# Kernel tuning notes

Measured on AMD Instinct MI355X. Metric: run time of the kernel, lower is better.

The kernel has to match this reference:

```python
import jax, jax.numpy as jnp
import numpy as np

N = 16384
H = 2048
E = 8
I_PER_E = 8192 // E  # expert_intermediate_size = 1024


def setup_inputs() -> dict:
    key = jax.random.key(0)
    k1, k2, k3, k4 = jax.random.split(key, 4)
    hidden_states = jax.random.normal(k1, (N, H), dtype=jnp.float32)
    # sort_idx is a permutation of [0, N): tokens sorted by expert assignment
    sort_idx = jax.random.permutation(k2, N).astype(jnp.int64)
    # kaiming_uniform_ with a=sqrt(5): bound = sqrt(6/((1+a^2)*fan_in)) = 1/sqrt(fan_in)
    bound = 1.0 / np.sqrt(H)
    gate_up_proj = jax.random.uniform(k3, (E, H, 2 * I_PER_E), dtype=jnp.float32,
                                      minval=-bound, maxval=bound)
    # original inits down_proj to zeros; use small random so backward is non-trivial
    down_proj = jax.random.normal(k4, (E, I_PER_E, H), dtype=jnp.float32) * 0.02
    return {"hidden_states": hidden_states, "sort_idx": sort_idx,
            "gate_up_proj": gate_up_proj, "down_proj": down_proj}


def reference(hidden_states, sort_idx, gate_up_proj, down_proj):
    n, h = hidden_states.shape
    e = gate_up_proj.shape[0]
    chunk = n // e
    # gather tokens into expert order: [E, chunk, H]
    sorted_x = hidden_states[sort_idx].reshape(e, chunk, h)
    # fused gate+up grouped GEMM: [E, chunk, 2*I/E]
    gu = jnp.einsum('ech,ehf->ecf', sorted_x, gate_up_proj)
    gate, up = jnp.split(gu, 2, axis=-1)
    activated = jax.nn.silu(gate) * up  # [E, chunk, I/E]
    sorted_out = jnp.einsum('eci,eih->ech', activated, down_proj).reshape(n, h)
    # scatter back: out[sort_idx] = sorted_out
    out = jnp.zeros((n, h), dtype=sorted_out.dtype).at[sort_idx].set(sorted_out)
    return out
```

## Files before the change

### kernel.cpp

```cpp
#include <hip/hip_runtime.h>
#include <hip/hip_bf16.h>

#define N_TOK 16384
#define H_DIM 2048
#define NE 8
#define CHUNK 2048
#define IPE 1024
#define F2 2048

typedef __bf16 bf16;
typedef bf16 bf16x8 __attribute__((ext_vector_type(8)));
typedef float f32x4 __attribute__((ext_vector_type(4)));

typedef __attribute__((address_space(1))) void gvoid;
typedef __attribute__((address_space(3))) void svoid;

__device__ __forceinline__ void gload_lds16(const void* g, void* l) {
  __builtin_amdgcn_global_load_lds((gvoid*)g, (svoid*)l, 16, 0, 0);
}
__device__ __forceinline__ f32x4 MF(bf16x8 a, bf16x8 b, f32x4 c) {
  return __builtin_amdgcn_mfma_f32_16x16x32_bf16(a, b, c, 0, 0, 0);
}

#define BAR() __builtin_amdgcn_s_barrier()
#define LGKM0() asm volatile("s_waitcnt lgkmcnt(0)" ::: "memory")
#define LGKM8() asm volatile("s_waitcnt lgkmcnt(8)" ::: "memory")
#define VM6() asm volatile("s_waitcnt vmcnt(6)" ::: "memory")
#define VM0() asm volatile("s_waitcnt vmcnt(0)" ::: "memory")
#define PRIO(x) __builtin_amdgcn_s_setprio(x)

__global__ __launch_bounds__(256) void k_gather(
    const float* __restrict__ x, const int* __restrict__ sidx,
    bf16* __restrict__ xs) {
  int row = blockIdx.x;
  int src = sidx[row];
  const float4* ip = (const float4*)(x + (size_t)src * H_DIM);
  int t = threadIdx.x;
  float4 f0 = ip[t * 2], f1 = ip[t * 2 + 1];
  bf16x8 v;
  v[0] = (bf16)f0.x; v[1] = (bf16)f0.y; v[2] = (bf16)f0.z; v[3] = (bf16)f0.w;
  v[4] = (bf16)f1.x; v[5] = (bf16)f1.y; v[6] = (bf16)f1.z; v[7] = (bf16)f1.w;
  *(bf16x8*)(xs + (size_t)row * H_DIM + t * 8) = v;
}

__global__ __launch_bounds__(256) void k_tr_w1(const float* __restrict__ in,
                                               bf16* __restrict__ out) {
  int e = blockIdx.z;
  int fB = blockIdx.x;
  int hB = blockIdx.y;
  __shared__ bf16 lds[64][68];
  int tx = threadIdx.x & 63;
  int ty = threadIdx.x >> 6;
  const float* ip = in + ((size_t)e * H_DIM + hB * 64) * F2;
  int scol = (tx < 32) ? (fB * 32 + tx) : (1024 + fB * 32 + (tx - 32));
#pragma unroll
  for (int p = 0; p < 16; ++p) {
    int hl = p * 4 + ty;
    lds[hl][tx] = (bf16)ip[(size_t)hl * F2 + scol];
  }
  __syncthreads();
  bf16* op = out + ((size_t)e * F2 + fB * 64) * H_DIM + hB * 64;
#pragma unroll
  for (int p = 0; p < 16; ++p) {
    int fl = p * 4 + ty;
    int g = fl >> 4, w = fl & 15;
    int lcol = ((g >> 1) << 4) + w + ((g & 1) << 5);
    op[(size_t)fl * H_DIM + tx] = lds[tx][lcol];
  }
}

__global__ __launch_bounds__(256) void k_tr_w2(const float* __restrict__ in,
                                               bf16* __restrict__ out) {
  int e = blockIdx.z;
  int hB = blockIdx.x;
  int iB = blockIdx.y;
  __shared__ bf16 lds[64][68];
  int tx = threadIdx.x & 63;
  int ty = threadIdx.x >> 6;
  const float* ip = in + (size_t)e * IPE * H_DIM + (size_t)iB * 64 * H_DIM + hB * 64;
#pragma unroll
  for (int p = 0; p < 16; ++p) {
    int il = p * 4 + ty;
    lds[il][tx] = (bf16)ip[(size_t)il * H_DIM + tx];
  }
  __syncthreads();
  bf16* op = out + (size_t)e * H_DIM * IPE + (size_t)hB * 64 * IPE + iB * 64;
#pragma unroll
  for (int p = 0; p < 16; ++p) {
    int hl = p * 4 + ty;
    op[(size_t)hl * IPE + tx] = lds[tx][hl];
  }
}

template <int KDIM, bool SILU>
__global__ __launch_bounds__(512) void k_gemm8(
    const bf16* __restrict__ Aptr, const bf16* __restrict__ Bptr,
    const int* __restrict__ sidx, bf16* __restrict__ act,
    float* __restrict__ fout) {
  extern __shared__ char smem[];
  const int tid = threadIdx.x, lane = tid & 63, wv = tid >> 6;
  const int wm = wv >> 2, wn = wv & 3;
  constexpr int NT = KDIM / 64;

  int swzwg = (blockIdx.x & 7) * (gridDim.x >> 3) + (blockIdx.x >> 3);
  const int e = swzwg >> 6, bm = (swzwg >> 3) & 7, bn = swzwg & 7;

  const char* Ab = (const char*)(Aptr + ((size_t)e * CHUNK + bm * 256) * KDIM);
  const char* Bb = (const char*)(Bptr + ((size_t)e * 2048 + bn * 256) * KDIM);

  const int L0 = wv * 1024 + lane * 16;
  const int lin0 = L0 ^ (((L0 >> 7) & 7) << 4);
  const int srow0 = lin0 >> 7, scolb = lin0 & 127;

  const int rA = lane & 15;
  const int swzr = (rA & 7) << 4;
  const int cb = (lane >> 4) * 16;

  f32x4 acc[8][4] = {};

  auto stage = [&](int buf, int mat, int half, int kt) {
    const char* gb = (mat == 0) ? Ab : Bb;
    char* ld = smem + buf * 65536 + mat * 32768 + half * 16384 + wv * 1024;
    size_t rb = (size_t)(half * 128 + srow0) * (KDIM * 2) + (size_t)kt * 128 + scolb;
    gload_lds16(gb + rb, ld);
    gload_lds16(gb + rb + (size_t)64 * (KDIM * 2), ld + 8192);
  };
  auto ldA = [&](int buf, int mi, int ks) {
    int lin = ((mi * 16 + rA) << 7) + ks * 64 + cb;
    return *(const bf16x8*)(smem + buf * 65536 + wm * 16384 + (lin ^ swzr));
  };
  auto ldB = [&](int buf, int ni, int ks) {
    int lin = (((wn & 1) * 64 + ni * 16 + rA) << 7) + ks * 64 + cb;
    return *(const bf16x8*)(smem + buf * 65536 + 32768 + (wn >> 1) * 16384 + (lin ^ swzr));
  };

  stage(0, 1, 0, 0); stage(0, 1, 1, 0); stage(0, 0, 0, 0); stage(0, 0, 1, 0);
  stage(1, 1, 0, 1); stage(1, 1, 1, 1); stage(1, 0, 0, 1);
  VM6();
  BAR();

  for (int t = 0; t < NT; ++t) {
    const int cur = t & 1, nxt = cur ^ 1;
    bf16x8 b0[4], b1[4], a0[4], a1[4], a2[4];
#pragma unroll
    for (int ni = 0; ni < 4; ++ni) { b0[ni] = ldB(cur, ni, 0); b1[ni] = ldB(cur, ni, 1); }
#pragma unroll
    for (int mi = 0; mi < 4; ++mi) a0[mi] = ldA(cur, mi, 0);
    if (t + 1 < NT) stage(nxt, 0, 1, t + 1);
    LGKM8();
    BAR();
    LGKM0();
    PRIO(1);
#pragma unroll
    for (int mi = 0; mi < 4; ++mi)
#pragma unroll
      for (int ni = 0; ni < 4; ++ni) acc[mi][ni] = MF(a0[mi], b0[ni], acc[mi][ni]);
    PRIO(0);
    BAR();
#pragma unroll
    for (int mi = 0; mi < 4; ++mi) a1[mi] = ldA(cur, mi, 1);
#pragma unroll
    for (int mi = 0; mi < 4; ++mi) a2[mi] = ldA(cur, 4 + mi, 0);
    if (t + 2 < NT) stage(cur, 1, 0, t + 2);
    BAR();
    LGKM0();
    PRIO(1);
#pragma unroll
    for (int mi = 0; mi < 4; ++mi)
#pragma unroll
      for (int ni = 0; ni < 4; ++ni) acc[mi][ni] = MF(a1[mi], b1[ni], acc[mi][ni]);
    PRIO(0);
    BAR();
#pragma unroll
    for (int mi = 0; mi < 4; ++mi) a0[mi] = ldA(cur, 4 + mi, 1);
    if (t + 2 < NT) stage(cur, 1, 1, t + 2);
    BAR();
    LGKM0();
    PRIO(1);
#pragma unroll
    for (int mi = 0; mi < 4; ++mi)
#pragma unroll
      for (int ni = 0; ni < 4; ++ni) acc[4 + mi][ni] = MF(a2[mi], b0[ni], acc[4 + mi][ni]);
    PRIO(0);
    BAR();
    if (t + 2 < NT) {
      stage(cur, 0, 0, t + 2);
      VM6();
    } else if (t + 1 < NT) {
      VM0();
    }
    BAR();
    PRIO(1);
#pragma unroll
    for (int mi = 0; mi < 4; ++mi)
#pragma unroll
      for (int ni = 0; ni < 4; ++ni) acc[4 + mi][ni] = MF(a0[mi], b1[ni], acc[4 + mi][ni]);
    PRIO(0);
    BAR();
  }

  if constexpr (SILU) {
    bf16* actp = act + ((size_t)e * CHUNK + bm * 256 + wm * 128) * IPE;
    const int r0 = (lane >> 4) * 4;
    const int c0 = bn * 128 + wn * 32 + (lane & 15);
#pragma unroll
    for (int mi = 0; mi < 8; ++mi)
#pragma unroll
      for (int p = 0; p < 2; ++p) {
        f32x4 g = acc[mi][2 * p], u = acc[mi][2 * p + 1];
#pragma unroll
        for (int r = 0; r < 4; ++r) {
          float gv = g[r];
          float a = gv / (1.f + __expf(-gv)) * u[r];
          actp[(size_t)(mi * 16 + r0 + r) * IPE + c0 + p * 16] = (bf16)a;
        }
      }
  } else {
    const int* sp = sidx + e * CHUNK + bm * 256 + wm * 128;
    const int r0 = (lane >> 4) * 4;
    const int c0 = bn * 256 + wn * 64 + (lane & 15);
#pragma unroll
    for (int mi = 0; mi < 8; ++mi)
#pragma unroll
      for (int r = 0; r < 4; ++r) {
        int dst = sp[mi * 16 + r0 + r];
        float* op = fout + (size_t)dst * H_DIM + c0;
#pragma unroll
        for (int ni = 0; ni < 4; ++ni) op[ni * 16] = acc[mi][ni][r];
      }
  }
}

extern "C" void kernel_launch(void* const* d_in, const int* in_sizes, int n_in,
                              void* d_out, int out_size, void* d_ws, size_t ws_size,
                              hipStream_t stream) {
  const float* hidden = (const float*)d_in[0];
  const int* sidx = (const int*)d_in[1];
  const float* w1 = (const float*)d_in[2];
  const float* w2 = (const float*)d_in[3];
  float* out = (float*)d_out;

  char* ws = (char*)d_ws;
  bf16* xs  = (bf16*)(ws);
  bf16* w1t = (bf16*)(ws + (size_t)67108864);
  bf16* act = (bf16*)(ws + (size_t)134217728);
  bf16* w2t = (bf16*)(ws);

  hipFuncSetAttribute((const void*)k_gemm8<H_DIM, true>,
                      hipFuncAttributeMaxDynamicSharedMemorySize, 131072);
  hipFuncSetAttribute((const void*)k_gemm8<IPE, false>,
                      hipFuncAttributeMaxDynamicSharedMemorySize, 131072);

  k_gather<<<dim3(N_TOK), 256, 0, stream>>>(hidden, sidx, xs);
  k_tr_w1<<<dim3(32, 32, NE), 256, 0, stream>>>(w1, w1t);
  k_gemm8<H_DIM, true><<<dim3(512), 512, 131072, stream>>>(xs, w1t, nullptr, act, nullptr);
  k_tr_w2<<<dim3(32, 16, NE), 256, 0, stream>>>(w2, w2t);
  k_gemm8<IPE, false><<<dim3(512), 512, 131072, stream>>>(act, w2t, sidx, nullptr, out);
}
```

Measured before the change: 305.9 us.

## Restructure GEMM inner loop to halve fragment registers and target two blocks per CU

After: 307.0 us. Within noise of the previous version (+0.4%).

```diff
diff --git a/kernel.cpp b/kernel.cpp
--- a/kernel.cpp
+++ b/kernel.cpp
@@ -28,6 +28,7 @@
 #define VM6() asm volatile("s_waitcnt vmcnt(6)" ::: "memory")
 #define VM0() asm volatile("s_waitcnt vmcnt(0)" ::: "memory")
 #define PRIO(x) __builtin_amdgcn_s_setprio(x)
+#define SCHED0() __builtin_amdgcn_sched_barrier(0)
 
 __global__ __launch_bounds__(256) void k_gather(
     const float* __restrict__ x, const int* __restrict__ sidx,
@@ -93,7 +94,7 @@
 }
 
 template <int KDIM, bool SILU>
-__global__ __launch_bounds__(512) void k_gemm8(
+__global__ __launch_bounds__(512, 2) void k_gemm8(
     const bf16* __restrict__ Aptr, const bf16* __restrict__ Bptr,
     const int* __restrict__ sidx, bf16* __restrict__ act,
     float* __restrict__ fout) {
@@ -139,48 +140,70 @@
   VM6();
   BAR();
 
-  for (int t = 0; t < NT; ++t) {
-    const int cur = t & 1, nxt = cur ^ 1;
-    bf16x8 b0[4], b1[4], a0[4], a1[4], a2[4];
-#pragma unroll
-    for (int ni = 0; ni < 4; ++ni) { b0[ni] = ldB(cur, ni, 0); b1[ni] = ldB(cur, ni, 1); }
-#pragma unroll
-    for (int mi = 0; mi < 4; ++mi) a0[mi] = ldA(cur, mi, 0);
+  auto ktile = [&](int t, int cur) {
+    const int nxt = cur ^ 1;
+    bf16x8 AA[4][2], B0[2][2], B1[2][2];
+#pragma unroll
+    for (int mi = 0; mi < 4; ++mi) {
+      AA[mi][0] = ldA(cur, mi, 0);
+      AA[mi][1] = ldA(cur, mi, 1);
+    }
+#pragma unroll
+    for (int ni = 0; ni < 2; ++ni) {
+      B0[ni][0] = ldB(cur, ni, 0);
+      B0[ni][1] = ldB(cur, ni, 1);
+    }
     if (t + 1 < NT) stage(nxt, 0, 1, t + 1);
     LGKM8();
     BAR();
     LGKM0();
-    PRIO(1);
-#pragma unroll
-    for (int mi = 0; mi < 4; ++mi)
-#pragma unroll
-      for (int ni = 0; ni < 4; ++ni) acc[mi][ni] = MF(a0[mi], b0[ni], acc[mi][ni]);
-    PRIO(0);
-    BAR();
-#pragma unroll
-    for (int mi = 0; mi < 4; ++mi) a1[mi] = ldA(cur, mi, 1);
-#pragma unroll
-    for (int mi = 0; mi < 4; ++mi) a2[mi] = ldA(cur, 4 + mi, 0);
+    SCHED0();
+    PRIO(1);
+#pragma unroll
+    for (int mi = 0; mi < 4; ++mi)
+#pragma unroll
+      for (int ni = 0; ni < 2; ++ni) {
+        acc[mi][ni] = MF(AA[mi][0], B0[ni][0], acc[mi][ni]);
+        acc[mi][ni] = MF(AA[mi][1], B0[ni][1], acc[mi][ni]);
+      }
+    PRIO(0);
+    BAR();
+#pragma unroll
+    for (int ni = 0; ni < 2; ++ni) {
+      B1[ni][0] = ldB(cur, 2 + ni, 0);
+      B1[ni][1] = ldB(cur, 2 + ni, 1);
+    }
     if (t + 2 < NT) stage(cur, 1, 0, t + 2);
     BAR();
     LGKM0();
-    PRIO(1);
-#pragma unroll
-    for (int mi = 0; mi < 4; ++mi)
-#pragma unroll
-      for (int ni = 0; ni < 4; ++ni) acc[mi][ni] = MF(a1[mi], b1[ni], acc[mi][ni]);
-    PRIO(0);
-    BAR();
-#pragma unroll
-    for (int mi = 0; mi < 4; ++mi) a0[mi] = ldA(cur, 4 + mi, 1);
+    SCHED0();
+    PRIO(1);
+#pragma unroll
+    for (int mi = 0; mi < 4; ++mi)
+#pragma unroll
+      for (int ni = 0; ni < 2; ++ni) {
+        acc[mi][2 + ni] = MF(AA[mi][0], B1[ni][0], acc[mi][2 + ni]);
+        acc[mi][2 + ni] = MF(AA[mi][1], B1[ni][1], acc[mi][2 + ni]);
+      }
+    PRIO(0);
+    BAR();
+#pragma unroll
+    for (int mi = 0; mi < 4; ++mi) {
+      AA[mi][0] = ldA(cur, 4 + mi, 0);
+      AA[mi][1] = ldA(cur, 4 + mi, 1);
+    }
     if (t + 2 < NT) stage(cur, 1, 1, t + 2);
     BAR();
     LGKM0();
-    PRIO(1);
-#pragma unroll
-    for (int mi = 0; mi < 4; ++mi)
-#pragma unroll
-      for (int ni = 0; ni < 4; ++ni) acc[4 + mi][ni] = MF(a2[mi], b0[ni], acc[4 + mi][ni]);
+    SCHED0();
+    PRIO(1);
+#pragma unroll
+    for (int mi = 0; mi < 4; ++mi)
+#pragma unroll
+      for (int ni = 0; ni < 2; ++ni) {
+        acc[4 + mi][ni] = MF(AA[mi][0], B0[ni][0], acc[4 + mi][ni]);
+        acc[4 + mi][ni] = MF(AA[mi][1], B0[ni][1], acc[4 + mi][ni]);
+      }
     PRIO(0);
     BAR();
     if (t + 2 < NT) {
@@ -194,9 +217,17 @@
 #pragma unroll
     for (int mi = 0; mi < 4; ++mi)
 #pragma unroll
-      for (int ni = 0; ni < 4; ++ni) acc[4 + mi][ni] = MF(a0[mi], b1[ni], acc[4 + mi][ni]);
-    PRIO(0);
-    BAR();
+      for (int ni = 0; ni < 2; ++ni) {
+        acc[4 + mi][2 + ni] = MF(AA[mi][0], B1[ni][0], acc[4 + mi][2 + ni]);
+        acc[4 + mi][2 + ni] = MF(AA[mi][1], B1[ni][1], acc[4 + mi][2 + ni]);
+      }
+    PRIO(0);
+    BAR();
+  };
+
+  for (int tt = 0; tt < NT; tt += 2) {
+    ktile(tt, 0);
+    ktile(tt + 1, 1);
   }
 
   if constexpr (SILU) {
```
